# Optimization experiments

Hardware: AMD Instinct MI355X
Metric: run time of the kernel (lower is better)

Reference implementation:

```python
import jax, jax.numpy as jnp
import numpy as np
import math

INPUT_WIDTH = 1024
KEY_WIDTH = 64
VALUE_WIDTH = 64
NUM_HEADS = 16
NUM_GROUPS = 4
HEADS_PER_GROUP = NUM_HEADS // NUM_GROUPS  # w = 4


def setup_inputs() -> dict:
    key = jax.random.key(0)
    k_x, k_q, k_k, k_v, k_p = jax.random.split(key, 5)
    n, s = 2, 2048
    # torch.nn.Linear weights are [out, in]; we store transposed [in, out] for x @ W.
    def lin(k, fan_in, fan_out):
        bound = 1.0 / math.sqrt(fan_in)
        return jax.random.uniform(k, (fan_in, fan_out), minval=-bound, maxval=bound, dtype=jnp.float32)
    return {
        "X": jax.random.normal(k_x, (n, s, INPUT_WIDTH), dtype=jnp.float32),
        "Wq": lin(k_q, INPUT_WIDTH, NUM_HEADS * KEY_WIDTH),
        "Wk": lin(k_k, INPUT_WIDTH, NUM_GROUPS * KEY_WIDTH),
        "Wv": lin(k_v, INPUT_WIDTH, NUM_GROUPS * VALUE_WIDTH),
        "Wpost": lin(k_p, NUM_HEADS * VALUE_WIDTH, INPUT_WIDTH),
    }


def reference(X, Wq, Wk, Wv, Wpost):
    n, s, _ = X.shape
    # Projections (no bias)
    Q = (X @ Wq).reshape(n, s, NUM_GROUPS, HEADS_PER_GROUP, KEY_WIDTH)  # [b,s,g,w,e]
    K = (X @ Wk).reshape(n, s, NUM_GROUPS, KEY_WIDTH)                   # [b,t,g,e]
    V = (X @ Wv).reshape(n, s, NUM_GROUPS, VALUE_WIDTH)                 # [b,t,g,e]
    scale = 1.0 / math.sqrt(KEY_WIDTH)
    # Grouped cross-attention: scores [b,s,t,g,w]
    raw = jnp.einsum('bsgwe,btge->bstgw', Q, K * scale)
    attn = jax.nn.softmax(raw, axis=2)  # softmax over key positions t
    A = jnp.einsum('bstgw,btge->bsgwe', attn, V).reshape(n, s, NUM_HEADS * VALUE_WIDTH)
    P = A @ Wpost
    return X + P
```

## Files before the change

kernel.cpp:

```cpp
#include <hip/hip_runtime.h>
#include <hip/hip_bf16.h>
#include <hip/hip_fp16.h>
#include <math.h>

typedef __attribute__((ext_vector_type(8))) short bfrag8;
typedef __attribute__((ext_vector_type(8))) _Float16 hfrag8;
typedef __attribute__((ext_vector_type(4))) float facc4;
typedef __attribute__((ext_vector_type(16))) float facc16;

#define MFMA16B(a, b, c) __builtin_amdgcn_mfma_f32_16x16x32_bf16((a), (b), (c), 0, 0, 0)
#define MFMA32B(a, b, c) __builtin_amdgcn_mfma_f32_32x32x16_bf16((a), (b), (c), 0, 0, 0)
#define MFMA32H(a, b, c) __builtin_amdgcn_mfma_f32_32x32x16_f16((a), (b), (c), 0, 0, 0)

__device__ __forceinline__ void gload_lds16(const void* g, void* l) {
    __builtin_amdgcn_global_load_lds(
        (const __attribute__((address_space(1))) void*)g,
        (__attribute__((address_space(3))) void*)l, 16, 0, 0);
}

__device__ __forceinline__ unsigned short f2bf(float f) {
    unsigned u = __float_as_uint(f);
    u += 0x7fffu + ((u >> 16) & 1u);
    return (unsigned short)(u >> 16);
}

__device__ __forceinline__ unsigned pk2(float a, float b) {
    auto h = __builtin_amdgcn_cvt_pkrtz(a, b);
    union { decltype(h) h; unsigned u; } c;
    c.h = h;
    return c.u;
}

__device__ __forceinline__ void do_transpose(const float* __restrict__ src,
                                             unsigned short* __restrict__ dst,
                                             int Kdim, int N, int nb, int kb,
                                             float (*tile)[33], int tid) {
    int tx = tid & 31, ty = tid >> 5;
#pragma unroll
    for (int r = ty; r < 32; r += 8)
        tile[r][tx] = src[(size_t)(kb + r) * N + nb + tx];
    __syncthreads();
#pragma unroll
    for (int r = ty; r < 32; r += 8)
        dst[(size_t)(nb + r) * Kdim + kb + tx] = f2bf(tile[tx][r]);
}

__global__ __launch_bounds__(256) void k_prep(
    const float* __restrict__ X, const float* __restrict__ Wq,
    const float* __restrict__ Wk, const float* __restrict__ Wv,
    const float* __restrict__ Wp,
    unsigned short* __restrict__ Xb, unsigned short* __restrict__ Wqkvt,
    unsigned short* __restrict__ Wpt) {
    __shared__ float tile[32][33];
    int blk = blockIdx.x, tid = threadIdx.x;
    if (blk < 4096) {
        int i = (blk * 256 + tid) * 4;
        float4 v = *reinterpret_cast<const float4*>(X + i);
        unsigned short o[4] = {f2bf(v.x), f2bf(v.y), f2bf(v.z), f2bf(v.w)};
        *reinterpret_cast<ulonglong1*>(Xb + i) = *reinterpret_cast<ulonglong1*>(o);
    } else if (blk < 5120) {
        int idx = blk - 4096;
        do_transpose(Wq, Wqkvt, 1024, 1024, (idx & 31) * 32, (idx >> 5) * 32, tile, tid);
    } else if (blk < 5376) {
        int idx = blk - 5120;
        do_transpose(Wk, Wqkvt + 1024 * 1024, 1024, 256, (idx & 7) * 32, (idx >> 3) * 32, tile, tid);
    } else if (blk < 5632) {
        int idx = blk - 5376;
        do_transpose(Wv, Wqkvt + 1280 * 1024, 1024, 256, (idx & 7) * 32, (idx >> 3) * 32, tile, tid);
    } else {
        int idx = blk - 5632;
        do_transpose(Wp, Wpt, 1024, 1024, (idx & 31) * 32, (idx >> 5) * 32, tile, tid);
    }
}

template <int EPI>
__global__ __launch_bounds__(256) void k_gemm_bt(
    const unsigned short* __restrict__ A, const unsigned short* __restrict__ Bt,
    int M, int N, int K,
    unsigned short* __restrict__ Qo, unsigned short* __restrict__ Ko,
    unsigned short* __restrict__ Vto,
    const float* __restrict__ Xres, float* __restrict__ Out) {
    __shared__ unsigned short Alds[128 * 64];
    __shared__ unsigned short Blds[128 * 64];
    const int tid = threadIdx.x;
    const int lane = tid & 63, wid = tid >> 6;
    const int wr = wid >> 1, wc = wid & 1;
    const int l15 = lane & 15, lhi = lane >> 4;
    const int m0 = blockIdx.y * 128, n0 = blockIdx.x * 128;

    facc4 acc[4][4] = {};

    for (int k0 = 0; k0 < K; k0 += 64) {
        __syncthreads();
#pragma unroll
        for (int i = 0; i < 4; ++i) {
            int seg = wid * 4 + i;
            int p = seg * 1024 + lane * 16;
            int row = p >> 7;
            int src = (p & 127) ^ ((row & 7) << 4);
            gload_lds16(A + (size_t)(m0 + row) * K + k0 + (src >> 1),
                        (char*)Alds + seg * 1024);
            gload_lds16(Bt + (size_t)(n0 + row) * K + k0 + (src >> 1),
                        (char*)Blds + seg * 1024);
        }
        __syncthreads();
#pragma unroll
        for (int kc = 0; kc < 2; ++kc) {
            bfrag8 af[4], bfv[4];
#pragma unroll
            for (int mi = 0; mi < 4; ++mi) {
                int row = wr * 64 + mi * 16 + l15;
                int off = (row * 128 + kc * 64 + lhi * 16) ^ ((row & 7) << 4);
                af[mi] = *reinterpret_cast<const bfrag8*>((const char*)Alds + off);
            }
#pragma unroll
            for (int ni = 0; ni < 4; ++ni) {
                int row = wc * 64 + ni * 16 + l15;
                int off = (row * 128 + kc * 64 + lhi * 16) ^ ((row & 7) << 4);
                bfv[ni] = *reinterpret_cast<const bfrag8*>((const char*)Blds + off);
            }
#pragma unroll
            for (int mi = 0; mi < 4; ++mi)
#pragma unroll
                for (int ni = 0; ni < 4; ++ni)
                    acc[mi][ni] = MFMA16B(af[mi], bfv[ni], acc[mi][ni]);
        }
    }

#pragma unroll
    for (int mi = 0; mi < 4; ++mi)
#pragma unroll
        for (int ni = 0; ni < 4; ++ni)
#pragma unroll
            for (int r = 0; r < 4; ++r) {
                int grow = m0 + wr * 64 + mi * 16 + lhi * 4 + r;
                int gcol = n0 + wc * 64 + ni * 16 + l15;
                float v = acc[mi][ni][r];
                if (EPI == 0) {
                    int b = grow >> 11, t = grow & 2047;
                    if (gcol < 1024) {
                        Qo[(size_t)grow * 1024 + gcol] = f2bf(v * 0.18033688f);
                    } else if (gcol < 1280) {
                        int cc = gcol - 1024;
                        int g = cc >> 6, e = cc & 63;
                        Ko[(((size_t)(b * 4 + g) * 2048 + t) << 6) + e] = f2bf(v);
                    } else {
                        int cc = gcol - 1280;
                        int g = cc >> 6, e = cc & 63;
                        Vto[((size_t)(b * 4 + g) * 64 + e) * 2048 + t] =
                            __half_as_ushort(__float2half(v));
                    }
                } else {
                    size_t idx = (size_t)grow * 1024 + gcol;
                    Out[idx] = Xres[idx] + v;
                }
            }
}

__global__ __launch_bounds__(512, 4) void k_attn(
    const unsigned short* __restrict__ Q,
    const unsigned short* __restrict__ Kb,
    const unsigned short* __restrict__ Vt,
    unsigned short* __restrict__ Abuf) {
    __shared__ char smem[65536];

    const int tid = threadIdx.x;
    const int lane = tid & 63, wid = tid >> 6;
    const int kvh = wid >> 2, qw = wid & 3;
    const int l31 = lane & 31, hi = lane >> 5;

    int wg = blockIdx.x;
    int swz = ((wg & 7) << 6) | (wg >> 3);
    const int qt = swz & 15, head = (swz >> 4) & 15, b = swz >> 8;
    const int g = head >> 2;
    const size_t kvK = (size_t)(b * 4 + g) * 2048 * 64;
    const size_t kvV = (size_t)(b * 4 + g) * 64 * 2048;
    const int qrow0 = b * 2048 + qt * 128 + qw * 32;

    bfrag8 qf[4];
#pragma unroll
    for (int ks = 0; ks < 4; ++ks)
        qf[ks] = *reinterpret_cast<const bfrag8*>(
            Q + (size_t)(qrow0 + l31) * 1024 + head * 64 + ks * 16 + hi * 8);

    const unsigned short* src[4];
    int ldsoff[4];
#pragma unroll
    for (int j = 0; j < 4; ++j) {
        int seg = (qw << 1) + (j & 1);
        bool isV = j >= 2;
        int p = seg * 1024 + lane * 16;
        int row = p >> 7;
        int sb = (p & 127) ^ ((row & 7) << 4);
        src[j] = !isV ? Kb + kvK + (size_t)(kvh * 64 + row) * 64 + (sb >> 1)
                      : Vt + kvV + (size_t)row * 2048 + kvh * 64 + (sb >> 1);
        ldsoff[j] = (isV ? 32768 : 0) + kvh * 16384 + seg * 1024;
    }

    facc16 o[2] = {};
    float psA = 0.f, psB = 0.f;

#pragma unroll
    for (int j = 0; j < 4; ++j) gload_lds16(src[j], smem + ldsoff[j]);
    __syncthreads();

    for (int t = 0; t < 16; ++t) {
        const int cur = t & 1;
        if (t < 15) {
#pragma unroll
            for (int j = 0; j < 4; ++j)
                gload_lds16(src[j] + (size_t)(t + 1) * (j < 2 ? 128 * 64 : 128),
                            smem + ldsoff[j] + (cur ^ 1) * 8192);
        }
        const char* Kc = smem + kvh * 16384 + cur * 8192;
        const char* Vc = smem + 32768 + kvh * 16384 + cur * 8192;

        facc16 s[2] = {};
        __builtin_amdgcn_s_setprio(1);
#pragma unroll
        for (int ks = 0; ks < 4; ++ks)
#pragma unroll
            for (int nt = 0; nt < 2; ++nt) {
                int row = nt * 32 + l31;
                int off = (row * 128 + ks * 32 + hi * 16) ^ ((row & 7) << 4);
                bfrag8 kf = *reinterpret_cast<const bfrag8*>(Kc + off);
                s[nt] = MFMA32B(kf, qf[ks], s[nt]);
            }
        __builtin_amdgcn_s_setprio(0);

#pragma unroll
        for (int nt = 0; nt < 2; ++nt) {
#pragma unroll
            for (int e = 0; e < 16; e += 2) {
                float e0 = __builtin_amdgcn_exp2f(s[nt][e]);
                float e1 = __builtin_amdgcn_exp2f(s[nt][e + 1]);
                s[nt][e] = e0;
                s[nt][e + 1] = e1;
                psA += e0;
                psB += e1;
            }
#pragma unroll
            for (int kh = 0; kh < 2; ++kh) {
                const int ks = nt * 2 + kh;
                const int pb = kh * 2;
                unsigned a0 = pk2(s[nt][4 * pb + 0], s[nt][4 * pb + 1]);
                unsigned a1 = pk2(s[nt][4 * pb + 2], s[nt][4 * pb + 3]);
                unsigned b0 = pk2(s[nt][4 * pb + 4], s[nt][4 * pb + 5]);
                unsigned b1 = pk2(s[nt][4 * pb + 6], s[nt][4 * pb + 7]);
                asm("v_permlane32_swap_b32 %0, %1" : "+v"(a0), "+v"(b0));
                asm("v_permlane32_swap_b32 %0, %1" : "+v"(a1), "+v"(b1));
                union { unsigned u[4]; hfrag8 h; } pu;
                pu.u[0] = a0; pu.u[1] = a1; pu.u[2] = b0; pu.u[3] = b1;
#pragma unroll
                for (int ot = 0; ot < 2; ++ot) {
                    int row = ot * 32 + l31;
                    int off = (row * 128 + ks * 32 + hi * 16) ^ ((row & 7) << 4);
                    hfrag8 vf = *reinterpret_cast<const hfrag8*>(Vc + off);
                    o[ot] = MFMA32H(vf, pu.h, o[ot]);
                }
            }
        }
        __syncthreads();
    }

    float psum = psA + psB;
    float* cmO = (float*)smem;
    float* cmL = (float*)(smem + 32768);
    if (kvh == 1) {
#pragma unroll
        for (int ot = 0; ot < 2; ++ot)
#pragma unroll
            for (int r = 0; r < 16; ++r)
                cmO[qw * 2048 + (ot * 16 + r) * 64 + lane] = o[ot][r];
        cmL[qw * 64 + lane] = psum;
    }
    __syncthreads();
    if (kvh == 0) {
#pragma unroll
        for (int ot = 0; ot < 2; ++ot)
#pragma unroll
            for (int r = 0; r < 16; ++r)
                o[ot][r] += cmO[qw * 2048 + (ot * 16 + r) * 64 + lane];
        psum += cmL[qw * 64 + lane];

        float l = psum + __shfl_xor(psum, 32, 64);
        float rl = 1.0f / l;
        int arow = qrow0 + l31;
#pragma unroll
        for (int ot = 0; ot < 2; ++ot)
#pragma unroll
            for (int p = 0; p < 4; ++p) {
                unsigned long long u = 0;
#pragma unroll
                for (int r = 0; r < 4; ++r)
                    u |= (unsigned long long)f2bf(o[ot][4 * p + r] * rl) << (16 * r);
                *reinterpret_cast<unsigned long long*>(
                    Abuf + (size_t)arow * 1024 + head * 64 + ot * 32 + p * 8 + hi * 4) = u;
            }
    }
}


extern "C" void kernel_launch(void* const* d_in, const int* in_sizes, int n_in,
                              void* d_out, int out_size, void* d_ws, size_t ws_size,
                              hipStream_t stream) {
    const float* X = (const float*)d_in[0];
    const float* Wq = (const float*)d_in[1];
    const float* Wk = (const float*)d_in[2];
    const float* Wv = (const float*)d_in[3];
    const float* Wpost = (const float*)d_in[4];
    float* Out = (float*)d_out;

    unsigned short* Xb = (unsigned short*)d_ws;
    unsigned short* Wqkvt = Xb + 4096 * 1024;
    unsigned short* Wpt = Wqkvt + 1536 * 1024;
    unsigned short* Qb = Wpt + 1024 * 1024;
    unsigned short* Kbuf = Qb + 4096 * 1024;
    unsigned short* Vtbuf = Kbuf + 8 * 2048 * 64;
    unsigned short* Abuf = Vtbuf + 8 * 2048 * 64;

    k_prep<<<6656, 256, 0, stream>>>(X, Wq, Wk, Wv, Wpost, Xb, Wqkvt, Wpt);

    k_gemm_bt<0><<<dim3(12, 32), 256, 0, stream>>>(Xb, Wqkvt, 4096, 1536, 1024,
                                                   Qb, Kbuf, Vtbuf, nullptr, nullptr);

    k_attn<<<512, 512, 0, stream>>>(Qb, Kbuf, Vtbuf, Abuf);

    k_gemm_bt<1><<<dim3(8, 32), 256, 0, stream>>>(Abuf, Wpt, 4096, 1024, 1024,
                                                  nullptr, nullptr, nullptr, X, Out);
}
```

Before: 107.6 us.

## Double-buffer GEMM LDS tiles with 512 threads and coalesce V transpose store

The projection GEMMs move to 512-thread blocks (8 waves, each holding a 64x32 output tile) and double-buffer the A/B LDS tiles, so the load of the next K slice overlaps MFMA work on the current one. The V-projection epilogue stages transposed fp16 results in LDS and writes them as coalesced 16-byte stores instead of scattered 2-byte strided writes. The attention kernel raises wave priority around its PV MFMA section. This adds LDS use (64KB per block) and lowers per-wave register reuse, which may limit how many blocks fit on a CU.

```diff
diff --git a/kernel.cpp b/kernel.cpp
--- a/kernel.cpp
+++ b/kernel.cpp
@@ -74,81 +74,115 @@
 }
 
 template <int EPI>
-__global__ __launch_bounds__(256) void k_gemm_bt(
+__global__ __launch_bounds__(512) void k_gemm_bt(
     const unsigned short* __restrict__ A, const unsigned short* __restrict__ Bt,
     int M, int N, int K,
     unsigned short* __restrict__ Qo, unsigned short* __restrict__ Ko,
     unsigned short* __restrict__ Vto,
     const float* __restrict__ Xres, float* __restrict__ Out) {
-    __shared__ unsigned short Alds[128 * 64];
-    __shared__ unsigned short Blds[128 * 64];
+    __shared__ char lds[65536];
     const int tid = threadIdx.x;
     const int lane = tid & 63, wid = tid >> 6;
-    const int wr = wid >> 1, wc = wid & 1;
+    const int wr = wid >> 2, wc = wid & 3;
     const int l15 = lane & 15, lhi = lane >> 4;
     const int m0 = blockIdx.y * 128, n0 = blockIdx.x * 128;
-
-    facc4 acc[4][4] = {};
-
-    for (int k0 = 0; k0 < K; k0 += 64) {
-        __syncthreads();
-#pragma unroll
-        for (int i = 0; i < 4; ++i) {
-            int seg = wid * 4 + i;
-            int p = seg * 1024 + lane * 16;
+    const int nk = K >> 6;
+
+    facc4 acc[4][2] = {};
+
+    int segbase = wid * 2;
+    int p0 = segbase * 1024 + lane * 16;
+
+    auto STAGE = [&](int buf, int k0) {
+#pragma unroll
+        for (int i = 0; i < 2; ++i) {
+            int p = p0 + i * 1024;
             int row = p >> 7;
             int src = (p & 127) ^ ((row & 7) << 4);
             gload_lds16(A + (size_t)(m0 + row) * K + k0 + (src >> 1),
-                        (char*)Alds + seg * 1024);
+                        lds + buf * 16384 + (segbase + i) * 1024);
             gload_lds16(Bt + (size_t)(n0 + row) * K + k0 + (src >> 1),
-                        (char*)Blds + seg * 1024);
+                        lds + 32768 + buf * 16384 + (segbase + i) * 1024);
         }
-        __syncthreads();
+    };
+
+    STAGE(0, 0);
+    __syncthreads();
+
+    for (int t = 0; t < nk; ++t) {
+        const int cur = t & 1;
+        if (t + 1 < nk) STAGE(cur ^ 1, (t + 1) * 64);
+        const char* Ab = lds + cur * 16384;
+        const char* Bb = lds + 32768 + cur * 16384;
 #pragma unroll
         for (int kc = 0; kc < 2; ++kc) {
-            bfrag8 af[4], bfv[4];
+            bfrag8 af[4], bfv[2];
 #pragma unroll
             for (int mi = 0; mi < 4; ++mi) {
                 int row = wr * 64 + mi * 16 + l15;
                 int off = (row * 128 + kc * 64 + lhi * 16) ^ ((row & 7) << 4);
-                af[mi] = *reinterpret_cast<const bfrag8*>((const char*)Alds + off);
-            }
-#pragma unroll
-            for (int ni = 0; ni < 4; ++ni) {
-                int row = wc * 64 + ni * 16 + l15;
+                af[mi] = *reinterpret_cast<const bfrag8*>(Ab + off);
+            }
+#pragma unroll
+            for (int ni = 0; ni < 2; ++ni) {
+                int row = wc * 32 + ni * 16 + l15;
                 int off = (row * 128 + kc * 64 + lhi * 16) ^ ((row & 7) << 4);
-                bfv[ni] = *reinterpret_cast<const bfrag8*>((const char*)Blds + off);
+                bfv[ni] = *reinterpret_cast<const bfrag8*>(Bb + off);
             }
 #pragma unroll
             for (int mi = 0; mi < 4; ++mi)
 #pragma unroll
-                for (int ni = 0; ni < 4; ++ni)
+                for (int ni = 0; ni < 2; ++ni)
                     acc[mi][ni] = MFMA16B(af[mi], bfv[ni], acc[mi][ni]);
         }
+        __syncthreads();
+    }
+
+    if (EPI == 0 && n0 >= 1280) {
+        unsigned short* VT = (unsigned short*)lds;
+#pragma unroll
+        for (int mi = 0; mi < 4; ++mi)
+#pragma unroll
+            for (int ni = 0; ni < 2; ++ni) {
+                int col = wc * 32 + ni * 16 + l15;
+                int row0 = wr * 64 + mi * 16 + lhi * 4;
+                unsigned long long u = 0;
+#pragma unroll
+                for (int r = 0; r < 4; ++r)
+                    u |= (unsigned long long)__half_as_ushort(__float2half(acc[mi][ni][r]))
+                         << (16 * r);
+                *reinterpret_cast<unsigned long long*>(VT + col * 136 + row0) = u;
+            }
+        __syncthreads();
+        int c = tid >> 2, q4 = tid & 3;
+        int b = m0 >> 11;
+        int g = ((n0 - 1280) >> 6) + (c >> 6);
+        int e = c & 63;
+        unsigned short* dstp = Vto + ((size_t)(b * 4 + g) * 64 + e) * 2048 + (m0 & 2047) + q4 * 32;
+        const unsigned short* srcp = VT + c * 136 + q4 * 32;
+#pragma unroll
+        for (int j = 0; j < 4; ++j)
+            *(reinterpret_cast<uint4*>(dstp) + j) = *(reinterpret_cast<const uint4*>(srcp) + j);
+        return;
     }
 
 #pragma unroll
     for (int mi = 0; mi < 4; ++mi)
 #pragma unroll
-        for (int ni = 0; ni < 4; ++ni)
+        for (int ni = 0; ni < 2; ++ni)
 #pragma unroll
             for (int r = 0; r < 4; ++r) {
                 int grow = m0 + wr * 64 + mi * 16 + lhi * 4 + r;
-                int gcol = n0 + wc * 64 + ni * 16 + l15;
+                int gcol = n0 + wc * 32 + ni * 16 + l15;
                 float v = acc[mi][ni][r];
                 if (EPI == 0) {
                     int b = grow >> 11, t = grow & 2047;
                     if (gcol < 1024) {
                         Qo[(size_t)grow * 1024 + gcol] = f2bf(v * 0.18033688f);
-                    } else if (gcol < 1280) {
+                    } else {
                         int cc = gcol - 1024;
                         int g = cc >> 6, e = cc & 63;
                         Ko[(((size_t)(b * 4 + g) * 2048 + t) << 6) + e] = f2bf(v);
-                    } else {
-                        int cc = gcol - 1280;
-                        int g = cc >> 6, e = cc & 63;
-                        Vto[((size_t)(b * 4 + g) * 64 + e) * 2048 + t] =
-                            __half_as_ushort(__float2half(v));
                     }
                 } else {
                     size_t idx = (size_t)grow * 1024 + gcol;
@@ -251,6 +285,7 @@
                 asm("v_permlane32_swap_b32 %0, %1" : "+v"(a1), "+v"(b1));
                 union { unsigned u[4]; hfrag8 h; } pu;
                 pu.u[0] = a0; pu.u[1] = a1; pu.u[2] = b0; pu.u[3] = b1;
+                __builtin_amdgcn_s_setprio(1);
 #pragma unroll
                 for (int ot = 0; ot < 2; ++ot) {
                     int row = ot * 32 + l31;
@@ -258,6 +293,7 @@
                     hfrag8 vf = *reinterpret_cast<const hfrag8*>(Vc + off);
                     o[ot] = MFMA32H(vf, pu.h, o[ot]);
                 }
+                __builtin_amdgcn_s_setprio(0);
             }
         }
         __syncthreads();
@@ -321,11 +357,11 @@
 
     k_prep<<<6656, 256, 0, stream>>>(X, Wq, Wk, Wv, Wpost, Xb, Wqkvt, Wpt);
 
-    k_gemm_bt<0><<<dim3(12, 32), 256, 0, stream>>>(Xb, Wqkvt, 4096, 1536, 1024,
+    k_gemm_bt<0><<<dim3(12, 32), 512, 0, stream>>>(Xb, Wqkvt, 4096, 1536, 1024,
                                                    Qb, Kbuf, Vtbuf, nullptr, nullptr);
 
     k_attn<<<512, 512, 0, stream>>>(Qb, Kbuf, Vtbuf, Abuf);
 
-    k_gemm_bt<1><<<dim3(8, 32), 256, 0, stream>>>(Abuf, Wpt, 4096, 1024, 1024,
+    k_gemm_bt<1><<<dim3(8, 32), 512, 0, stream>>>(Abuf, Wpt, 4096, 1024, 1024,
                                                   nullptr, nullptr, nullptr, X, Out);
 }
```

Measured after the change: 92.29 us. -14.2%, faster.
